# Kernel tuning notes

Hardware: AMD Instinct MI355X
Metric: run time of the kernel (lower is better)

Reference implementation:

```python
import jax, jax.numpy as jnp
import numpy as np

B, T, D, H = 4, 2048, 1024, 16
HD = D // H


def setup_inputs() -> dict:
    key = jax.random.key(0)
    kq, kk, kv, k1, k2, k3, k4 = jax.random.split(key, 7)
    q = jax.random.normal(kq, (B, T, D), dtype=jnp.float32)
    k = jax.random.normal(kk, (B, T, D), dtype=jnp.float32)
    v = jax.random.normal(kv, (B, T, D), dtype=jnp.float32)
    # causal mask, broadcast over heads: [B, 1, T, T]
    mask = jnp.broadcast_to(jnp.tril(jnp.ones((T, T), dtype=bool)), (B, 1, T, T))
    s = 0.02
    Wq = jax.random.normal(k1, (D, D), dtype=jnp.float32) * s
    Wk = jax.random.normal(k2, (D, D), dtype=jnp.float32) * s
    Wv = jax.random.normal(k3, (D, D), dtype=jnp.float32) * s
    Wo = jax.random.normal(k4, (D, D), dtype=jnp.float32) * s
    return {"q": q, "k": k, "v": v, "mask": mask,
            "Wq": Wq, "Wk": Wk, "Wv": Wv, "Wo": Wo}


def reference(q, k, v, mask, Wq, Wk, Wv, Wo):
    scale = HD ** -0.5
    # nn.Linear: y = x @ W.T  (bias=False)
    qh = (q @ Wq.T).reshape(B, T, H, HD).transpose(0, 2, 1, 3)  # [B,H,T,HD]
    kh = (k @ Wk.T).reshape(B, -1, H, HD).transpose(0, 2, 1, 3)
    vh = (v @ Wv.T).reshape(B, -1, H, HD).transpose(0, 2, 1, 3)
    scores = jnp.einsum('bhqd,bhkd->bhqk', qh, kh) * scale  # [B,H,T,T]
    # dropout p=0.0 -> identity (applied pre-mask in original)
    scores = jnp.where(mask, scores, -jnp.inf)
    probs = jax.nn.softmax(scores, axis=-1)
    attn = jnp.einsum('bhqk,bhkd->bhqd', probs, vh)  # [B,H,T,HD]
    attn = attn.transpose(0, 2, 1, 3).reshape(B, T, D)
    return attn @ Wo.T
```

## Files before the change

kernel.cpp:

```cpp
#include <hip/hip_runtime.h>
#include <stdint.h>

#define B_  4
#define T_  2048
#define D_  1024
#define H_  16
#define HD_ 64
#define KK_ 1024

typedef __bf16 bf16_t;
typedef __bf16 bf16x8 __attribute__((ext_vector_type(8)));
typedef float  f32x4  __attribute__((ext_vector_type(4)));
typedef float  f32x16 __attribute__((ext_vector_type(16)));

__device__ __forceinline__ uint16_t f2bf(float f) {
  uint32_t x = __float_as_uint(f);
  uint32_t r = (x + 0x7fffu + ((x >> 16) & 1u)) >> 16;
  return (uint16_t)r;
}

__device__ __forceinline__ uint32_t pack2(float a, float b) {
  return (uint32_t)f2bf(a) | ((uint32_t)f2bf(b) << 16);
}

__device__ __forceinline__ float exp2a(float x) {
  float r;
  asm("v_exp_f32 %0, %1" : "=v"(r) : "v"(x));
  return r;
}

__device__ __forceinline__ uint32_t cvtpk(float a, float b) {
  uint32_t r;
  asm("v_cvt_pk_bf16_f32 %0, %1, %2" : "=v"(r) : "v"(a), "v"(b));
  return r;
}

__device__ __forceinline__ void plswap(uint32_t& a, uint32_t& b) {
  asm("v_permlane32_swap_b32 %0, %1" : "+v"(a), "+v"(b));
}

__device__ __forceinline__ void gll16(const void* g, void* l) {
  __builtin_amdgcn_global_load_lds(
      (const __attribute__((address_space(1))) void*)g,
      (__attribute__((address_space(3))) void*)l, 16, 0, 0);
}

__global__ __launch_bounds__(256) void cvtW(const float* __restrict__ s0,
                                            const float* __restrict__ s1,
                                            const float* __restrict__ s2,
                                            const float* __restrict__ s3,
                                            uint16_t* __restrict__ d0,
                                            uint16_t* __restrict__ d1,
                                            uint16_t* __restrict__ d2,
                                            uint16_t* __restrict__ d3) {
  const float* in = blockIdx.y == 0 ? s0 : (blockIdx.y == 1 ? s1 :
                    (blockIdx.y == 2 ? s2 : s3));
  uint16_t* out = blockIdx.y == 0 ? d0 : (blockIdx.y == 1 ? d1 :
                  (blockIdx.y == 2 ? d2 : d3));
  int i = (blockIdx.x * 256 + threadIdx.x) * 8;
  float4 a = *(const float4*)(in + i);
  float4 b = *(const float4*)(in + i + 4);
  uint4 u;
  u.x = pack2(a.x, a.y);
  u.y = pack2(a.z, a.w);
  u.z = pack2(b.x, b.y);
  u.w = pack2(b.z, b.w);
  *(uint4*)(out + i) = u;
}

template <bool AF32>
__global__ __launch_bounds__(512, 2)
void gemm8(const void* __restrict__ a0, const void* __restrict__ a1,
           const void* __restrict__ a2, const uint16_t* __restrict__ w0,
           const uint16_t* __restrict__ w1, const uint16_t* __restrict__ w2,
           void* __restrict__ o0, void* __restrict__ o1, void* __restrict__ o2,
           int mode_base, float scale0) {
  __shared__ __align__(16) uint16_t Ab[3][128 * 64];
  __shared__ __align__(16) uint16_t Bb[3][256 * 64];

  const int nwg = gridDim.x;
  const int bid = blockIdx.x;
  const int cpx = nwg >> 3;
  const int swz = (bid & 7) * cpx + (bid >> 3);
  const int g = swz >> 8;
  const int r = swz & 255;
  const int mt = r >> 2, nt = r & 3;
  const int m0 = mt * 128, n0 = nt * 256;

  const void* A = g == 0 ? a0 : (g == 1 ? a1 : a2);
  const uint16_t* W = g == 0 ? w0 : (g == 1 ? w1 : w2);
  void* Out = g == 0 ? o0 : (g == 1 ? o1 : o2);
  const int mode = mode_base + g;
  const float scale = (mode == 0) ? scale0 : 1.0f;
  const float* A32 = (const float*)A;
  const uint16_t* A16 = (const uint16_t*)A;

  const int tid = threadIdx.x;
  const int wid = tid >> 6, lane = tid & 63;
  const int fr = lane & 15, fq = lane >> 4;
  const int wm = wid >> 2, wn = wid & 3;
  const int srow = lane >> 3, c8 = lane & 7;

  f32x4 acc[4][4];
#pragma unroll
  for (int i = 0; i < 4; ++i)
#pragma unroll
    for (int j = 0; j < 4; ++j) acc[i][j] = (f32x4){0.f, 0.f, 0.f, 0.f};

  const int NT = KK_ / 64;
  float4 ax[4];

#define AISSUE(bi, t)                                                         \
  do {                                                                        \
    if (AF32) {                                                               \
      _Pragma("unroll")                                                       \
      for (int c = 0; c < 2; ++c) {                                           \
        int row = c * 64 + wid * 8 + srow;                                    \
        int sw = (c8 ^ (row & 7)) << 3;                                       \
        const float* src = A32 + (size_t)(m0 + row) * KK_ + (t) * 64 + sw;    \
        ax[c * 2] = *(const float4*)src;                                      \
        ax[c * 2 + 1] = *(const float4*)(src + 4);                            \
      }                                                                       \
    } else {                                                                  \
      _Pragma("unroll")                                                       \
      for (int c = 0; c < 2; ++c) {                                           \
        int row = c * 64 + wid * 8 + srow;                                    \
        int sw = (c8 ^ (row & 7)) << 3;                                       \
        gll16(A16 + (size_t)(m0 + row) * KK_ + (t) * 64 + sw,                 \
              &Ab[bi][c * 4096 + wid * 512]);                                 \
      }                                                                       \
    }                                                                         \
  } while (0)

#define AWRITE(bi)                                                            \
  do {                                                                        \
    if (AF32) {                                                               \
      _Pragma("unroll")                                                       \
      for (int c = 0; c < 2; ++c) {                                           \
        uint4 u;                                                              \
        u.x = cvtpk(ax[c * 2].x, ax[c * 2].y);                                \
        u.y = cvtpk(ax[c * 2].z, ax[c * 2].w);                                \
        u.z = cvtpk(ax[c * 2 + 1].x, ax[c * 2 + 1].y);                        \
        u.w = cvtpk(ax[c * 2 + 1].z, ax[c * 2 + 1].w);                        \
        *(uint4*)&Ab[bi][c * 4096 + wid * 512 + lane * 8] = u;                \
      }                                                                       \
    }                                                                         \
  } while (0)

#define STAGEB(bi, t)                                                         \
  do {                                                                        \
    _Pragma("unroll")                                                         \
    for (int c = 0; c < 4; ++c) {                                             \
      int row = c * 64 + wid * 8 + srow;                                      \
      int sw = (c8 ^ (row & 7)) << 3;                                         \
      gll16(W + (size_t)(n0 + row) * KK_ + (t) * 64 + sw,                     \
            &Bb[bi][c * 4096 + wid * 512]);                                   \
    }                                                                         \
  } while (0)

  AISSUE(0, 0);
  STAGEB(0, 0);
  if (AF32) {
    asm volatile("s_waitcnt vmcnt(4)" ::: "memory");
    AWRITE(0);
  }
  AISSUE(1, 1);
  STAGEB(1, 1);
  if (AF32) {
    asm volatile("s_waitcnt vmcnt(4)" ::: "memory");
    AWRITE(1);
  } else {
    asm volatile("s_waitcnt vmcnt(6)" ::: "memory");
  }
  asm volatile("s_waitcnt lgkmcnt(0)" ::: "memory");
  __builtin_amdgcn_s_barrier();

  int cur = 0;
  for (int t = 0; t < NT; ++t) {
    const uint16_t* Ac = &Ab[cur][0];
    const uint16_t* Bc = &Bb[cur][0];
    int nb = cur + 2; if (nb >= 3) nb -= 3;
    if (t + 2 < NT) {
      AISSUE(nb, t + 2);
      STAGEB(nb, t + 2);
    }
    bf16x8 af0[4], bf0[4];
#pragma unroll
    for (int i = 0; i < 4; ++i) {
      int ra = wm * 64 + i * 16 + fr;
      af0[i] = *(const bf16x8*)&Ac[ra * 64 + ((fq ^ (ra & 7)) << 3)];
      int rb = wn * 64 + i * 16 + fr;
      bf0[i] = *(const bf16x8*)&Bc[rb * 64 + ((fq ^ (rb & 7)) << 3)];
    }
    bf16x8 af1[4], bf1[4];
#pragma unroll
    for (int i = 0; i < 4; ++i) {
      int ra = wm * 64 + i * 16 + fr;
      af1[i] = *(const bf16x8*)&Ac[ra * 64 + (((4 + fq) ^ (ra & 7)) << 3)];
      int rb = wn * 64 + i * 16 + fr;
      bf1[i] = *(const bf16x8*)&Bc[rb * 64 + (((4 + fq) ^ (rb & 7)) << 3)];
    }
    __builtin_amdgcn_s_setprio(1);
#pragma unroll
    for (int mf = 0; mf < 4; ++mf)
#pragma unroll
      for (int nf = 0; nf < 4; ++nf)
        acc[mf][nf] = __builtin_amdgcn_mfma_f32_16x16x32_bf16(af0[mf], bf0[nf],
                                                              acc[mf][nf], 0, 0, 0);
#pragma unroll
    for (int mf = 0; mf < 4; ++mf)
#pragma unroll
      for (int nf = 0; nf < 4; ++nf)
        acc[mf][nf] = __builtin_amdgcn_mfma_f32_16x16x32_bf16(af1[mf], bf1[nf],
                                                              acc[mf][nf], 0, 0, 0);
    __builtin_amdgcn_s_setprio(0);
    if (t + 2 < NT) {
      if (AF32) {
        asm volatile("s_waitcnt vmcnt(4)" ::: "memory");
        AWRITE(nb);
      } else {
        asm volatile("s_waitcnt vmcnt(6)" ::: "memory");
      }
    } else if (t + 1 < NT) {
      asm volatile("s_waitcnt vmcnt(0)" ::: "memory");
    }
    if (t + 1 < NT) {
      asm volatile("s_waitcnt lgkmcnt(0)" ::: "memory");
      __builtin_amdgcn_s_barrier();
    }
    ++cur; if (cur == 3) cur = 0;
  }
#undef AISSUE
#undef AWRITE
#undef STAGEB

#pragma unroll
  for (int mf = 0; mf < 4; ++mf) {
#pragma unroll
    for (int nf = 0; nf < 4; ++nf) {
      int m = m0 + wm * 64 + mf * 16 + fq * 4;
      int n = n0 + wn * 64 + nf * 16 + fr;
      if (mode == 2) {
        int b = m >> 11, t = m & (T_ - 1);
        int h = n >> 6, hd = n & 63;
        uint2 pk;
        pk.x = pack2(acc[mf][nf][0], acc[mf][nf][1]);
        pk.y = pack2(acc[mf][nf][2], acc[mf][nf][3]);
        uint16_t* dst = (uint16_t*)Out + ((((size_t)b * H_ + h) * HD_ + hd) * T_ + t);
        *(uint2*)dst = pk;
      } else if (mode == 3) {
#pragma unroll
        for (int rr = 0; rr < 4; ++rr)
          ((float*)Out)[(size_t)(m + rr) * D_ + n] = acc[mf][nf][rr];
      } else {
#pragma unroll
        for (int rr = 0; rr < 4; ++rr) {
          int mm = m + rr;
          int b = mm >> 11, t = mm & (T_ - 1);
          int h = n >> 6, hd = n & 63;
          ((uint16_t*)Out)[((((size_t)b * H_ + h) * T_ + t) << 6) + hd] =
              f2bf(acc[mf][nf][rr] * scale);
        }
      }
    }
  }
}

__global__ __launch_bounds__(512)
void attn_fwd(const uint16_t* __restrict__ Qh, const uint16_t* __restrict__ Kh,
              const uint16_t* __restrict__ Vt, uint16_t* __restrict__ O) {
  __shared__ __align__(16) uint16_t SB[6][64 * 64];

  const int tid = threadIdx.x, wid = tid >> 6, lane = tid & 63;
  const int ql = lane & 31, hi = lane >> 5;
  const int bid = blockIdx.x;
  const int qb = (T_ / 256 - 1) - (bid >> 6);
  const int bh = bid & 63;
  const int q0 = qb * 256;
  const int wq0 = q0 + wid * 32;
  const size_t hoff = (size_t)bh * T_ * HD_;
  const uint16_t* Qp = Qh + hoff;
  const uint16_t* Kp = Kh + hoff;
  const uint16_t* Vp = Vt + hoff;

  bf16x8 qf[4];
  {
    const uint16_t* qrow = Qp + (size_t)(wq0 + ql) * 64 + hi * 8;
#pragma unroll
    for (int ks = 0; ks < 4; ++ks) qf[ks] = *(const bf16x8*)(qrow + ks * 16);
  }

  float m = -1e30f, l = 0.f;
  f32x16 acc[2];
#pragma unroll
  for (int mo = 0; mo < 2; ++mo)
#pragma unroll
    for (int r = 0; r < 16; ++r) acc[mo][r] = 0.f;

  const int ntiles = 4 * qb + 4;

#define STAGE(buf, t)                                                        \
  do {                                                                       \
    int row = wid * 8 + (lane >> 3);                                         \
    int sw = ((lane & 7) ^ (row & 7)) << 3;                                  \
    gll16(Kp + (size_t)((t) * 64 + row) * 64 + sw, &SB[buf][wid * 512]);     \
    gll16(Vp + (size_t)row * T_ + (t) * 64 + sw, &SB[3 + (buf)][wid * 512]); \
  } while (0)

  STAGE(0, 0);
  if (ntiles > 1) STAGE(1, 1);
  asm volatile("s_waitcnt vmcnt(2)" ::: "memory");
  __builtin_amdgcn_s_barrier();

  int cur = 0;
  for (int it = 0; it < ntiles; ++it) {
    if (it + 2 < ntiles) {
      int nb = cur + 2; if (nb >= 3) nb -= 3;
      STAGE(nb, it + 2);
    }

    if (it * 64 <= wq0 + 31) {
      f32x16 st[2];
#pragma unroll
      for (int mm = 0; mm < 2; ++mm)
#pragma unroll
        for (int r = 0; r < 16; ++r) st[mm][r] = 0.f;
#pragma unroll
      for (int ks = 0; ks < 4; ++ks) {
#pragma unroll
        for (int mm = 0; mm < 2; ++mm) {
          int row = mm * 32 + ql;
          int ch = (ks * 2 + hi) ^ (row & 7);
          bf16x8 kf = *(const bf16x8*)&SB[cur][row * 64 + ch * 8];
          st[mm] = __builtin_amdgcn_mfma_f32_32x32x16_bf16(kf, qf[ks], st[mm], 0, 0, 0);
        }
      }

      if (it * 64 + 63 > wq0) {
        int qg = wq0 + ql;
#pragma unroll
        for (int mm = 0; mm < 2; ++mm)
#pragma unroll
          for (int r = 0; r < 16; ++r) {
            int kv = it * 64 + mm * 32 + (r & 3) + 8 * (r >> 2) + 4 * hi;
            if (kv > qg) st[mm][r] = -1e30f;
          }
      }

      float pm = st[0][0];
#pragma unroll
      for (int r = 1; r < 16; ++r) pm = fmaxf(pm, st[0][r]);
#pragma unroll
      for (int r = 0; r < 16; ++r) pm = fmaxf(pm, st[1][r]);
      pm = fmaxf(pm, __shfl_xor(pm, 32));

      if (__any(pm > m + 8.f)) {
        float mn = fmaxf(m, pm);
        float sf = exp2a(m - mn);
        m = mn;
        l *= sf;
#pragma unroll
        for (int mo = 0; mo < 2; ++mo)
#pragma unroll
          for (int r = 0; r < 16; ++r) acc[mo][r] *= sf;
      }

      float rs = 0.f;
#pragma unroll
      for (int mm = 0; mm < 2; ++mm)
#pragma unroll
        for (int r = 0; r < 16; ++r) {
          float p = exp2a(st[mm][r] - m);
          st[mm][r] = p;
          rs += p;
        }
      rs += __shfl_xor(rs, 32);
      l += rs;

      bf16x8 pf[4];
#pragma unroll
      for (int mm = 0; mm < 2; ++mm)
#pragma unroll
        for (int g = 0; g < 2; ++g) {
          uint32_t a1 = cvtpk(st[mm][8 * g + 0], st[mm][8 * g + 1]);
          uint32_t a2 = cvtpk(st[mm][8 * g + 2], st[mm][8 * g + 3]);
          uint32_t b1 = cvtpk(st[mm][8 * g + 4], st[mm][8 * g + 5]);
          uint32_t b2 = cvtpk(st[mm][8 * g + 6], st[mm][8 * g + 7]);
          plswap(a1, b1);
          plswap(a2, b2);
          union { uint32_t w[4]; bf16x8 v; } u;
          u.w[0] = a1; u.w[1] = a2; u.w[2] = b1; u.w[3] = b2;
          pf[mm * 2 + g] = u.v;
        }

#pragma unroll
      for (int ks = 0; ks < 4; ++ks) {
#pragma unroll
        for (int mo = 0; mo < 2; ++mo) {
          int row = mo * 32 + ql;
          int ch = (ks * 2 + hi) ^ (row & 7);
          bf16x8 vf = *(const bf16x8*)&SB[3 + cur][row * 64 + ch * 8];
          acc[mo] = __builtin_amdgcn_mfma_f32_32x32x16_bf16(vf, pf[ks], acc[mo], 0, 0, 0);
        }
      }
    }

    if (it + 1 < ntiles) {
      if (it + 2 < ntiles) {
        asm volatile("s_waitcnt vmcnt(2)" ::: "memory");
      } else {
        asm volatile("s_waitcnt vmcnt(0)" ::: "memory");
      }
      __builtin_amdgcn_s_barrier();
    }
    ++cur; if (cur == 3) cur = 0;
  }
#undef STAGE

  __syncthreads();
  uint16_t* ost = &SB[0][0];
  {
    float inv = 1.0f / l;
    uint16_t* wst = ost + wid * 2048;
#pragma unroll
    for (int mo = 0; mo < 2; ++mo)
#pragma unroll
      for (int r = 0; r < 16; r += 2) {
        int hd = mo * 32 + (r & 3) + 8 * (r >> 2) + 4 * hi;
        uint32_t pk = pack2(acc[mo][r] * inv, acc[mo][r + 1] * inv);
        int col = hd ^ ((ql & 7) << 3);
        *(uint32_t*)&wst[ql * 64 + col] = pk;
      }
  }
  __syncthreads();
  {
    int row = tid >> 1, half = tid & 1;
    int r7 = row & 7;
    int b = bh >> 4, h = bh & 15;
    size_t g = (size_t)(b * T_ + q0 + row) * D_ + h * 64 + half * 32;
#pragma unroll
    for (int j = 0; j < 4; ++j) {
      int cc = half * 4 + j;
      uint4 val = *(const uint4*)&ost[row * 64 + (cc ^ r7) * 8];
      *(uint4*)&O[g + j * 8] = val;
    }
  }
}

extern "C" void kernel_launch(void* const* d_in, const int* in_sizes, int n_in,
                              void* d_out, int out_size, void* d_ws, size_t ws_size,
                              hipStream_t stream) {
  (void)in_sizes; (void)n_in; (void)out_size; (void)ws_size;
  const float* q  = (const float*)d_in[0];
  const float* k  = (const float*)d_in[1];
  const float* v  = (const float*)d_in[2];
  const float* Wq = (const float*)d_in[4];
  const float* Wk = (const float*)d_in[5];
  const float* Wv = (const float*)d_in[6];
  const float* Wo = (const float*)d_in[7];

  uint8_t* ws = (uint8_t*)d_ws;
  const size_t MB = 1u << 20;
  uint16_t* WQB = (uint16_t*)(ws + 0 * MB);
  uint16_t* WKB = (uint16_t*)(ws + 2 * MB);
  uint16_t* WVB = (uint16_t*)(ws + 4 * MB);
  uint16_t* WOB = (uint16_t*)(ws + 6 * MB);
  uint16_t* QH  = (uint16_t*)(ws + 56 * MB);
  uint16_t* KH  = (uint16_t*)(ws + 72 * MB);
  uint16_t* VT  = (uint16_t*)(ws + 88 * MB);
  uint16_t* AC  = (uint16_t*)(ws + 8 * MB);

  cvtW<<<dim3(D_ * D_ / 2048, 4), 256, 0, stream>>>(Wq, Wk, Wv, Wo, WQB, WKB, WVB, WOB);

  const float qscale = 0.125f * 1.44269504088896340736f;

  gemm8<true><<<dim3(768), 512, 0, stream>>>(q, k, v, WQB, WKB, WVB,
                                             QH, KH, VT, 0, qscale);

  attn_fwd<<<dim3(T_ / 256 * 64), 512, 0, stream>>>(QH, KH, VT, AC);

  gemm8<false><<<dim3(256), 512, 0, stream>>>(AC, nullptr, nullptr,
                                              WOB, nullptr, nullptr,
                                              d_out, nullptr, nullptr, 3, 1.0f);
}
```

Baseline: 166.3 us.

## Double-buffer fp32 A register loads and move global issues after first LDS fragment reads

The GEMM main loop now keeps two register buffers for fp32 A tiles (ping-pong via a 2x unrolled BODY macro). The global loads for tile t+2 are issued after the first half of the LDS fragment reads. The bf16 conversion and LDS write of tile t+1 are deferred until after the MFMAs, so fp32 global loads get a full iteration of latency hiding instead of being waited on mid-iteration. This adds register pressure from the extra float4 buffers, which may reduce occupancy.

```diff
diff --git a/kernel.cpp b/kernel.cpp
--- a/kernel.cpp
+++ b/kernel.cpp
@@ -108,42 +108,41 @@
     for (int j = 0; j < 4; ++j) acc[i][j] = (f32x4){0.f, 0.f, 0.f, 0.f};
 
   const int NT = KK_ / 64;
-  float4 ax[4];
-
-#define AISSUE(bi, t)                                                         \
+  float4 axA[4], axB[4];
+
+#define ALOAD(ax, t)                                                          \
   do {                                                                        \
-    if (AF32) {                                                               \
-      _Pragma("unroll")                                                       \
-      for (int c = 0; c < 2; ++c) {                                           \
-        int row = c * 64 + wid * 8 + srow;                                    \
-        int sw = (c8 ^ (row & 7)) << 3;                                       \
-        const float* src = A32 + (size_t)(m0 + row) * KK_ + (t) * 64 + sw;    \
-        ax[c * 2] = *(const float4*)src;                                      \
-        ax[c * 2 + 1] = *(const float4*)(src + 4);                            \
-      }                                                                       \
-    } else {                                                                  \
-      _Pragma("unroll")                                                       \
-      for (int c = 0; c < 2; ++c) {                                           \
-        int row = c * 64 + wid * 8 + srow;                                    \
-        int sw = (c8 ^ (row & 7)) << 3;                                       \
-        gll16(A16 + (size_t)(m0 + row) * KK_ + (t) * 64 + sw,                 \
-              &Ab[bi][c * 4096 + wid * 512]);                                 \
-      }                                                                       \
-    }                                                                         \
-  } while (0)
-
-#define AWRITE(bi)                                                            \
+    _Pragma("unroll")                                                         \
+    for (int c = 0; c < 2; ++c) {                                             \
+      int row = c * 64 + wid * 8 + srow;                                      \
+      int sw = (c8 ^ (row & 7)) << 3;                                         \
+      const float* src = A32 + (size_t)(m0 + row) * KK_ + (t) * 64 + sw;      \
+      ax[c * 2] = *(const float4*)src;                                        \
+      ax[c * 2 + 1] = *(const float4*)(src + 4);                              \
+    }                                                                         \
+  } while (0)
+
+#define AWRITE(bi, ax)                                                        \
   do {                                                                        \
-    if (AF32) {                                                               \
-      _Pragma("unroll")                                                       \
-      for (int c = 0; c < 2; ++c) {                                           \
-        uint4 u;                                                              \
-        u.x = cvtpk(ax[c * 2].x, ax[c * 2].y);                                \
-        u.y = cvtpk(ax[c * 2].z, ax[c * 2].w);                                \
-        u.z = cvtpk(ax[c * 2 + 1].x, ax[c * 2 + 1].y);                        \
-        u.w = cvtpk(ax[c * 2 + 1].z, ax[c * 2 + 1].w);                        \
-        *(uint4*)&Ab[bi][c * 4096 + wid * 512 + lane * 8] = u;                \
-      }                                                                       \
+    _Pragma("unroll")                                                         \
+    for (int c = 0; c < 2; ++c) {                                             \
+      uint4 u;                                                                \
+      u.x = cvtpk(ax[c * 2].x, ax[c * 2].y);                                  \
+      u.y = cvtpk(ax[c * 2].z, ax[c * 2].w);                                  \
+      u.z = cvtpk(ax[c * 2 + 1].x, ax[c * 2 + 1].y);                          \
+      u.w = cvtpk(ax[c * 2 + 1].z, ax[c * 2 + 1].w);                          \
+      *(uint4*)&Ab[bi][c * 4096 + wid * 512 + srow * 64 + c8 * 8] = u;        \
+    }                                                                         \
+  } while (0)
+
+#define STAGEA16(bi, t)                                                       \
+  do {                                                                        \
+    _Pragma("unroll")                                                         \
+    for (int c = 0; c < 2; ++c) {                                             \
+      int row = c * 64 + wid * 8 + srow;                                      \
+      int sw = (c8 ^ (row & 7)) << 3;                                         \
+      gll16(A16 + (size_t)(m0 + row) * KK_ + (t) * 64 + sw,                   \
+            &Ab[bi][c * 4096 + wid * 512]);                                   \
     }                                                                         \
   } while (0)
 
@@ -158,80 +157,84 @@
     }                                                                         \
   } while (0)
 
-  AISSUE(0, 0);
-  STAGEB(0, 0);
   if (AF32) {
-    asm volatile("s_waitcnt vmcnt(4)" ::: "memory");
-    AWRITE(0);
-  }
-  AISSUE(1, 1);
-  STAGEB(1, 1);
-  if (AF32) {
-    asm volatile("s_waitcnt vmcnt(4)" ::: "memory");
-    AWRITE(1);
+    ALOAD(axA, 0);
+    STAGEB(0, 0);
+    AWRITE(0, axA);
+    ALOAD(axA, 1);
+    STAGEB(1, 1);
+    asm volatile("s_waitcnt vmcnt(8)" ::: "memory");
   } else {
+    STAGEA16(0, 0);
+    STAGEB(0, 0);
+    STAGEA16(1, 1);
+    STAGEB(1, 1);
     asm volatile("s_waitcnt vmcnt(6)" ::: "memory");
   }
   asm volatile("s_waitcnt lgkmcnt(0)" ::: "memory");
   __builtin_amdgcn_s_barrier();
 
+#define BODY(t, axU, axL)                                                     \
+  do {                                                                        \
+    const uint16_t* Ac = &Ab[cur][0];                                         \
+    const uint16_t* Bc = &Bb[cur][0];                                         \
+    int nb = cur + 2; if (nb >= 3) nb -= 3;                                   \
+    bf16x8 af0[4], bf0[4], af1[4], bf1[4];                                    \
+    _Pragma("unroll")                                                         \
+    for (int i = 0; i < 4; ++i) {                                             \
+      int ra = wm * 64 + i * 16 + fr;                                         \
+      af0[i] = *(const bf16x8*)&Ac[ra * 64 + ((fq ^ (ra & 7)) << 3)];         \
+      int rb = wn * 64 + i * 16 + fr;                                         \
+      bf0[i] = *(const bf16x8*)&Bc[rb * 64 + ((fq ^ (rb & 7)) << 3)];         \
+    }                                                                         \
+    if ((t) + 2 < NT) {                                                       \
+      if (AF32) { ALOAD(axL, (t) + 2); } else { STAGEA16(nb, (t) + 2); }      \
+      STAGEB(nb, (t) + 2);                                                    \
+    }                                                                         \
+    _Pragma("unroll")                                                         \
+    for (int i = 0; i < 4; ++i) {                                             \
+      int ra = wm * 64 + i * 16 + fr;                                         \
+      af1[i] = *(const bf16x8*)&Ac[ra * 64 + (((4 + fq) ^ (ra & 7)) << 3)];   \
+      int rb = wn * 64 + i * 16 + fr;                                         \
+      bf1[i] = *(const bf16x8*)&Bc[rb * 64 + (((4 + fq) ^ (rb & 7)) << 3)];   \
+    }                                                                         \
+    __builtin_amdgcn_s_setprio(1);                                            \
+    _Pragma("unroll")                                                         \
+    for (int mf = 0; mf < 4; ++mf)                                            \
+      _Pragma("unroll")                                                       \
+      for (int nf = 0; nf < 4; ++nf)                                          \
+        acc[mf][nf] = __builtin_amdgcn_mfma_f32_16x16x32_bf16(                \
+            af0[mf], bf0[nf], acc[mf][nf], 0, 0, 0);                          \
+    _Pragma("unroll")                                                         \
+    for (int mf = 0; mf < 4; ++mf)                                            \
+      _Pragma("unroll")                                                       \
+      for (int nf = 0; nf < 4; ++nf)                                          \
+        acc[mf][nf] = __builtin_amdgcn_mfma_f32_16x16x32_bf16(                \
+            af1[mf], bf1[nf], acc[mf][nf], 0, 0, 0);                          \
+    __builtin_amdgcn_s_setprio(0);                                            \
+    if ((t) + 1 < NT) {                                                       \
+      int wb = cur + 1; if (wb >= 3) wb -= 3;                                 \
+      if (AF32) AWRITE(wb, axU);          \
+      if ((t) + 2 < NT) {                                                     \
+        asm volatile("s_waitcnt vmcnt(%0)" ::"i"(AF32 ? 8 : 6) : "memory");   \
+      } else {                                                                \
+        asm volatile("s_waitcnt vmcnt(0)" ::: "memory");                      \
+      }                                                                       \
+      asm volatile("s_waitcnt lgkmcnt(0)" ::: "memory");                      \
+      __builtin_amdgcn_s_barrier();                                           \
+    }                                                                         \
+    ++cur; if (cur == 3) cur = 0;                                             \
+  } while (0)
+
   int cur = 0;
-  for (int t = 0; t < NT; ++t) {
-    const uint16_t* Ac = &Ab[cur][0];
-    const uint16_t* Bc = &Bb[cur][0];
-    int nb = cur + 2; if (nb >= 3) nb -= 3;
-    if (t + 2 < NT) {
-      AISSUE(nb, t + 2);
-      STAGEB(nb, t + 2);
-    }
-    bf16x8 af0[4], bf0[4];
-#pragma unroll
-    for (int i = 0; i < 4; ++i) {
-      int ra = wm * 64 + i * 16 + fr;
-      af0[i] = *(const bf16x8*)&Ac[ra * 64 + ((fq ^ (ra & 7)) << 3)];
-      int rb = wn * 64 + i * 16 + fr;
-      bf0[i] = *(const bf16x8*)&Bc[rb * 64 + ((fq ^ (rb & 7)) << 3)];
-    }
-    bf16x8 af1[4], bf1[4];
-#pragma unroll
-    for (int i = 0; i < 4; ++i) {
-      int ra = wm * 64 + i * 16 + fr;
-      af1[i] = *(const bf16x8*)&Ac[ra * 64 + (((4 + fq) ^ (ra & 7)) << 3)];
-      int rb = wn * 64 + i * 16 + fr;
-      bf1[i] = *(const bf16x8*)&Bc[rb * 64 + (((4 + fq) ^ (rb & 7)) << 3)];
-    }
-    __builtin_amdgcn_s_setprio(1);
-#pragma unroll
-    for (int mf = 0; mf < 4; ++mf)
-#pragma unroll
-      for (int nf = 0; nf < 4; ++nf)
-        acc[mf][nf] = __builtin_amdgcn_mfma_f32_16x16x32_bf16(af0[mf], bf0[nf],
-                                                              acc[mf][nf], 0, 0, 0);
-#pragma unroll
-    for (int mf = 0; mf < 4; ++mf)
-#pragma unroll
-      for (int nf = 0; nf < 4; ++nf)
-        acc[mf][nf] = __builtin_amdgcn_mfma_f32_16x16x32_bf16(af1[mf], bf1[nf],
-                                                              acc[mf][nf], 0, 0, 0);
-    __builtin_amdgcn_s_setprio(0);
-    if (t + 2 < NT) {
-      if (AF32) {
-        asm volatile("s_waitcnt vmcnt(4)" ::: "memory");
-        AWRITE(nb);
-      } else {
-        asm volatile("s_waitcnt vmcnt(6)" ::: "memory");
-      }
-    } else if (t + 1 < NT) {
-      asm volatile("s_waitcnt vmcnt(0)" ::: "memory");
-    }
-    if (t + 1 < NT) {
-      asm volatile("s_waitcnt lgkmcnt(0)" ::: "memory");
-      __builtin_amdgcn_s_barrier();
-    }
-    ++cur; if (cur == 3) cur = 0;
-  }
-#undef AISSUE
+  for (int tt = 0; tt < NT; tt += 2) {
+    BODY(tt, axA, axB);
+    BODY(tt + 1, axB, axA);
+  }
+#undef BODY
+#undef ALOAD
 #undef AWRITE
+#undef STAGEA16
 #undef STAGEB
 
 #pragma unroll
@@ -439,10 +442,10 @@
     int b = bh >> 4, h = bh & 15;
     size_t g = (size_t)(b * T_ + q0 + row) * D_ + h * 64 + half * 32;
 #pragma unroll
-    for (int j = 0; j < 4; ++j) {
-      int cc = half * 4 + j;
+    for (int j2 = 0; j2 < 4; ++j2) {
+      int cc = half * 4 + j2;
       uint4 val = *(const uint4*)&ost[row * 64 + (cc ^ r7) * 8];
-      *(uint4*)&O[g + j * 8] = val;
+      *(uint4*)&O[g + j2 * 8] = val;
     }
   }
 }
```

After: 165.8 us. No clear change (-0.3%).
